# Performance work log

Measured on AMD Instinct MI355X. Metric: run time of the kernel, lower is better.

## Reference

```python
import jax, jax.numpy as jnp
import numpy as np

H = 1024   # hidden size
E = 8      # num experts
B, S = 4, 2048


def setup_inputs() -> dict:
    key = jax.random.key(0)
    k1, k2, k3, k4 = jax.random.split(key, 4)
    x = jax.random.normal(k1, (B, S, H), dtype=jnp.float32)
    wg = jax.random.normal(k2, (H, E), dtype=jnp.float32) * 0.02      # gate weight
    W = jax.random.normal(k3, (E, H, H), dtype=jnp.float32) * 0.02    # expert Linear weights (out, in) per expert
    b = jax.random.normal(k4, (E, H), dtype=jnp.float32) * 0.02       # expert Linear biases
    return {"x": x, "wg": wg, "W": W, "b": b}


def reference(x, wg, W, b):
    Bb, Ss, Hh = x.shape
    Ee = wg.shape[1]
    T = Bb * Ss
    C = T // Ee  # capacity (capacity_factor = 1.0, top-1)

    xt = x.reshape(T, Hh)
    logits = xt @ wg                                   # [T, E]
    probs = jax.nn.softmax(logits, axis=-1)            # [T, E]
    idx = jnp.argmax(probs, axis=-1)                   # [T] top-1 expert
    mask = jax.nn.one_hot(idx, Ee, dtype=xt.dtype)     # [T, E]

    # position of each token within its expert's queue (0-based)
    locations = jnp.cumsum(mask, axis=0) - mask        # [T, E]
    # drop tokens over capacity
    mask = mask * (locations < C).astype(xt.dtype)
    gate = jnp.sum(probs * mask, axis=-1)              # [T] gate prob (0 if dropped)
    loc_s = jnp.sum(locations * mask, axis=-1).astype(jnp.int32)  # [T]
    loc_oh = jax.nn.one_hot(loc_s, C, dtype=xt.dtype)  # [T, C]

    dispatch = mask[:, :, None] * loc_oh[:, None, :]   # [T, E, C]
    combine = gate[:, None, None] * dispatch           # [T, E, C]

    # dispatch tokens -> per-expert buffers [E, C, H]
    exp_in = jnp.einsum('tec,th->ech', dispatch, xt)
    # per-expert Linear: y = x @ W_e^T + b_e
    exp_out = jnp.einsum('ech,efh->ecf', exp_in, W) + b[:, None, :]
    # combine back to tokens, scaled by gate prob
    out = jnp.einsum('tec,ecf->tf', combine, exp_out)  # [T, H]
    return out.reshape(Bb, Ss, Hh)
```

## Files before the change

kernel.cpp:

```cpp
#include <hip/hip_runtime.h>

#define H 1024
#define E 8
#define T 8192
#define CAP 1024

typedef __bf16 bf16x8 __attribute__((ext_vector_type(8)));
typedef float  f32x4  __attribute__((ext_vector_type(4)));
typedef unsigned short u16;

__device__ __forceinline__ u16 f2bf(float f) {
    union { float f; unsigned u; } v; v.f = f;
    unsigned r = v.u + 0x7FFFu + ((v.u >> 16) & 1u);
    return (u16)(r >> 16);
}

typedef __attribute__((address_space(1))) const void* gas_t;
typedef __attribute__((address_space(3))) void* las_t;
__device__ __forceinline__ void gld16(const void* g, void* l) {
    __builtin_amdgcn_global_load_lds((gas_t)g, (las_t)l, 16, 0, 0);
}

__global__ __launch_bounds__(256) void gate_kernel(
    const float* __restrict__ x, const float* __restrict__ wg,
    int* __restrict__ eid, float* __restrict__ gate, u16* __restrict__ xbf) {
    const int wave = (blockIdx.x * blockDim.x + threadIdx.x) >> 6;
    const int lane = threadIdx.x & 63;
    const float* xr = x + (size_t)wave * H;
    float acc[E];
    #pragma unroll
    for (int e = 0; e < E; ++e) acc[e] = 0.f;
    #pragma unroll
    for (int q = 0; q < H / 64; ++q) {
        const int h = q * 64 + lane;
        const float xv = xr[h];
        if (xbf) xbf[(size_t)wave * H + h] = f2bf(xv);
        const float* wr = wg + h * E;
        #pragma unroll
        for (int e = 0; e < E; ++e) acc[e] += xv * wr[e];
    }
    #pragma unroll
    for (int off = 32; off >= 1; off >>= 1) {
        #pragma unroll
        for (int e = 0; e < E; ++e) acc[e] += __shfl_xor(acc[e], off);
    }
    if (lane == 0) {
        float m = acc[0]; int best = 0;
        #pragma unroll
        for (int e = 1; e < E; ++e) if (acc[e] > m) { m = acc[e]; best = e; }
        float s = 0.f;
        #pragma unroll
        for (int e = 0; e < E; ++e) s += expf(acc[e] - m);
        eid[wave]  = best;
        gate[wave] = 1.0f / s;
    }
}

__global__ __launch_bounds__(256) void cvt_kernel(
    const float* __restrict__ src, u16* __restrict__ dst, int n4) {
    int i = blockIdx.x * blockDim.x + threadIdx.x;
    const int stride = gridDim.x * blockDim.x;
    for (; i < n4; i += stride) {
        float4 v = ((const float4*)src)[i];
        ushort4 o;
        o.x = f2bf(v.x); o.y = f2bf(v.y); o.z = f2bf(v.z); o.w = f2bf(v.w);
        ((ushort4*)dst)[i] = o;
    }
}

#define TPT 32
__global__ __launch_bounds__(256) void scan_kernel(
    const int* __restrict__ eid, float* __restrict__ gate,
    int* __restrict__ perm) {
    __shared__ int cnt[256][E];
    __shared__ int base[256][E];
    __shared__ int part[E][8];
    const int tid = threadIdx.x;

    for (int i = tid; i < E * CAP; i += 256) perm[i] = -1;

    const int t0 = tid * TPT;
    int c[E];
    #pragma unroll
    for (int e = 0; e < E; ++e) c[e] = 0;
    for (int i = 0; i < TPT; ++i) {
        const int ei = eid[t0 + i];
        #pragma unroll
        for (int e = 0; e < E; ++e) c[e] += (ei == e);
    }
    #pragma unroll
    for (int e = 0; e < E; ++e) cnt[tid][e] = c[e];
    __syncthreads();
    if (tid < 64) {
        const int e = tid >> 3, j = tid & 7;
        int s = 0;
        for (int i = j * 32; i < j * 32 + 32; ++i) s += cnt[i][e];
        part[e][j] = s;
    }
    __syncthreads();
    if (tid < E) {
        int run = 0;
        #pragma unroll
        for (int j = 0; j < 8; ++j) { int v = part[tid][j]; part[tid][j] = run; run += v; }
    }
    __syncthreads();
    if (tid < 64) {
        const int e = tid >> 3, j = tid & 7;
        int run = part[e][j];
        for (int i = j * 32; i < j * 32 + 32; ++i) { base[i][e] = run; run += cnt[i][e]; }
    }
    __syncthreads();
    #pragma unroll
    for (int e = 0; e < E; ++e) c[e] = base[tid][e];
    for (int i = 0; i < TPT; ++i) {
        const int t = t0 + i;
        const int ei = eid[t];
        int pos = 0;
        #pragma unroll
        for (int e = 0; e < E; ++e) if (ei == e) pos = c[e]++;
        if (pos < CAP) perm[ei * CAP + pos] = t;
        else gate[t] = 0.f;
    }
}

#define BK 64
__global__ __launch_bounds__(256) void moe_gemm_bf(
    const u16* __restrict__ xbf, const u16* __restrict__ Wbf,
    const float* __restrict__ bias, const int* __restrict__ perm,
    const float* __restrict__ gate, float* __restrict__ out) {
    __shared__ __align__(16) u16 As[128 * BK];
    __shared__ __align__(16) u16 Bs[128 * BK];
    __shared__ int   perm_s[128];
    __shared__ float gate_s[128];

    const int e   = blockIdx.z;
    const int mb  = blockIdx.y;
    const int fb  = blockIdx.x;
    const int tid = threadIdx.x;

    if (tid < 128) {
        const int t = perm[e * CAP + mb * 128 + tid];
        perm_s[tid] = t;
        gate_s[tid] = (t >= 0) ? gate[t] : 0.f;
    }
    __syncthreads();

    const int lane = tid & 63;
    const int wv = tid >> 6;
    const int wm = wv >> 1, wn = wv & 1;
    const int l16 = lane & 15, quad = lane >> 4;

    const int rl   = lane >> 3;
    const int cch  = lane & 7;
    const int gch  = cch ^ rl;
    const u16* ga[4]; const u16* gb[4];
    u16* la[4]; u16* lb[4];
    #pragma unroll
    for (int q = 0; q < 4; ++q) {
        const int r = (wv * 4 + q) * 8 + rl;
        const int tA = perm_s[r];
        const int tok = tA >= 0 ? tA : 0;
        ga[q] = xbf + (size_t)tok * H + gch * 8;
        gb[q] = Wbf + (size_t)e * H * H + (size_t)(fb * 128 + r) * H + gch * 8;
        la[q] = &As[(wv * 4 + q) * 512 + lane * 8];
        lb[q] = &Bs[(wv * 4 + q) * 512 + lane * 8];
    }

    f32x4 acc[4][4] = {};

    for (int kt = 0; kt < H / BK; ++kt) {
        __syncthreads();
        #pragma unroll
        for (int q = 0; q < 4; ++q) {
            gld16(ga[q], la[q]);
            gld16(gb[q], lb[q]);
            ga[q] += BK; gb[q] += BK;
        }
        __syncthreads();
        #pragma unroll
        for (int s = 0; s < 2; ++s) {
            bf16x8 af[4], bfr[4];
            const int cc = (s * 4 + quad) ^ (l16 & 7);
            #pragma unroll
            for (int i = 0; i < 4; ++i) {
                af[i]  = *(const bf16x8*)&As[(wm * 64 + i * 16 + l16) * BK + cc * 8];
                bfr[i] = *(const bf16x8*)&Bs[(wn * 64 + i * 16 + l16) * BK + cc * 8];
            }
            #pragma unroll
            for (int mi = 0; mi < 4; ++mi)
                #pragma unroll
                for (int ni = 0; ni < 4; ++ni)
                    acc[mi][ni] = __builtin_amdgcn_mfma_f32_16x16x32_bf16(
                        af[mi], bfr[ni], acc[mi][ni], 0, 0, 0);
        }
    }

    float bv[4];
    #pragma unroll
    for (int ni = 0; ni < 4; ++ni)
        bv[ni] = bias[e * H + fb * 128 + wn * 64 + ni * 16 + l16];

    #pragma unroll
    for (int mi = 0; mi < 4; ++mi) {
        #pragma unroll
        for (int r = 0; r < 4; ++r) {
            const int rowl = wm * 64 + mi * 16 + quad * 4 + r;
            const int t = perm_s[rowl];
            if (t < 0) continue;
            const float g = gate_s[rowl];
            float* orow = out + (size_t)t * H + fb * 128 + wn * 64;
            #pragma unroll
            for (int ni = 0; ni < 4; ++ni)
                orow[ni * 16 + l16] = g * (acc[mi][ni][r] + bv[ni]);
        }
    }
}

#define LDA 40
__global__ __launch_bounds__(256) void moe_gemm_f32(
    const float* __restrict__ x, const float* __restrict__ W,
    const float* __restrict__ bias, const int* __restrict__ perm,
    const float* __restrict__ gate, float* __restrict__ out) {
    __shared__ __align__(16) u16 As[128 * LDA];
    __shared__ __align__(16) u16 Bs[128 * LDA];
    __shared__ int   perm_s[128];
    __shared__ float gate_s[128];

    const int e   = blockIdx.z;
    const int mb  = blockIdx.y;
    const int fb  = blockIdx.x;
    const int tid = threadIdx.x;

    if (tid < 128) {
        const int t = perm[e * CAP + mb * 128 + tid];
        perm_s[tid] = t;
        gate_s[tid] = (t >= 0) ? gate[t] : 0.f;
    }
    __syncthreads();

    const int lane = tid & 63;
    const int wv = tid >> 6;
    const int wm = wv >> 1, wn = wv & 1;
    const int l16 = lane & 15, quad = lane >> 4;

    f32x4 acc[4][4] = {};
    const float* Wbase = W + (size_t)e * H * H + (size_t)(fb * 128) * H;

    for (int kt = 0; kt < H / 32; ++kt) {
        const int k0 = kt * 32;
        __syncthreads();
        #pragma unroll
        for (int p = 0; p < 4; ++p) {
            const int cidx = p * 256 + tid;
            const int row = cidx >> 3;
            const int col = (cidx & 7) * 4;
            const int t = perm_s[row];
            float4 va = (t >= 0) ? *(const float4*)(x + (size_t)t * H + k0 + col)
                                 : make_float4(0.f, 0.f, 0.f, 0.f);
            u16* da = &As[row * LDA + col];
            da[0] = f2bf(va.x); da[1] = f2bf(va.y); da[2] = f2bf(va.z); da[3] = f2bf(va.w);
            float4 vb = *(const float4*)(Wbase + (size_t)row * H + k0 + col);
            u16* db = &Bs[row * LDA + col];
            db[0] = f2bf(vb.x); db[1] = f2bf(vb.y); db[2] = f2bf(vb.z); db[3] = f2bf(vb.w);
        }
        __syncthreads();
        bf16x8 af[4], bfr[4];
        #pragma unroll
        for (int i = 0; i < 4; ++i) {
            af[i]  = *(const bf16x8*)&As[(wm * 64 + i * 16 + l16) * LDA + quad * 8];
            bfr[i] = *(const bf16x8*)&Bs[(wn * 64 + i * 16 + l16) * LDA + quad * 8];
        }
        #pragma unroll
        for (int mi = 0; mi < 4; ++mi)
            #pragma unroll
            for (int ni = 0; ni < 4; ++ni)
                acc[mi][ni] = __builtin_amdgcn_mfma_f32_16x16x32_bf16(
                    af[mi], bfr[ni], acc[mi][ni], 0, 0, 0);
    }

    float bv[4];
    #pragma unroll
    for (int ni = 0; ni < 4; ++ni)
        bv[ni] = bias[e * H + fb * 128 + wn * 64 + ni * 16 + l16];
    #pragma unroll
    for (int mi = 0; mi < 4; ++mi) {
        #pragma unroll
        for (int r = 0; r < 4; ++r) {
            const int rowl = wm * 64 + mi * 16 + quad * 4 + r;
            const int t = perm_s[rowl];
            if (t < 0) continue;
            const float g = gate_s[rowl];
            float* orow = out + (size_t)t * H + fb * 128 + wn * 64;
            #pragma unroll
            for (int ni = 0; ni < 4; ++ni)
                orow[ni * 16 + l16] = g * (acc[mi][ni][r] + bv[ni]);
        }
    }
}

__global__ __launch_bounds__(256) void zero_dropped(
    const float* __restrict__ gate, float* __restrict__ out) {
    const int wave = (blockIdx.x * blockDim.x + threadIdx.x) >> 6;
    const int lane = threadIdx.x & 63;
    if (gate[wave] != 0.f) return;
    float4 z = make_float4(0.f, 0.f, 0.f, 0.f);
    float4* o = (float4*)(out + (size_t)wave * H);
    #pragma unroll
    for (int i = 0; i < H / 4 / 64; ++i) o[i * 64 + lane] = z;
}

extern "C" void kernel_launch(void* const* d_in, const int* in_sizes, int n_in,
                              void* d_out, int out_size, void* d_ws, size_t ws_size,
                              hipStream_t stream) {
    const float* x    = (const float*)d_in[0];
    const float* wg   = (const float*)d_in[1];
    const float* W    = (const float*)d_in[2];
    const float* bias = (const float*)d_in[3];
    float* out = (float*)d_out;

    int*   eid  = (int*)d_ws;
    float* gate = (float*)((char*)d_ws + (size_t)T * 4);
    int*   perm = (int*)((char*)d_ws + (size_t)T * 8);
    u16*   xbf  = (u16*)((char*)d_ws + (size_t)T * 12);
    u16*   Wbf  = xbf + (size_t)T * H;
    const size_t need = (size_t)T * 12 + (size_t)T * H * 2 + (size_t)E * H * H * 2;
    const bool fast = ws_size >= need;

    gate_kernel<<<T / 4, 256, 0, stream>>>(x, wg, eid, gate, fast ? xbf : nullptr);
    if (fast) cvt_kernel<<<2048, 256, 0, stream>>>(W, Wbf, E * H * H / 4);
    scan_kernel<<<1, 256, 0, stream>>>(eid, gate, perm);
    if (fast)
        moe_gemm_bf<<<dim3(8, 8, 8), 256, 0, stream>>>(xbf, Wbf, bias, perm, gate, out);
    else
        moe_gemm_f32<<<dim3(8, 8, 8), 256, 0, stream>>>(x, W, bias, perm, gate, out);
    zero_dropped<<<T / 4, 256, 0, stream>>>(gate, out);
}
```

Measured before the change: 176.8 us.

## Fuse gating and weight conversion into one kernel with LDS-staged gate weights

Merges the gate/x-to-bf16 kernel and the W-to-bf16 conversion kernel into a single launch, with separate block ranges for each job. Gate blocks stage wg in shared memory, each wave processes four tokens with float4 loads, and the eight expert partial sums are reduced with a transpose-style shuffle scheme. The intent is to cut one launch, let the two memory-bound passes overlap, and make the gating loads more efficient. The fp32 fallback GEMM and the workspace-size check are removed, so the code now assumes the workspace is always large enough.

```diff
diff --git a/kernel.cpp b/kernel.cpp
--- a/kernel.cpp
+++ b/kernel.cpp
@@ -21,50 +21,107 @@
     __builtin_amdgcn_global_load_lds((gas_t)g, (las_t)l, 16, 0, 0);
 }
 
-__global__ __launch_bounds__(256) void gate_kernel(
+#define GATE_BLOCKS 512
+#define CVT_BLOCKS  1536
+#define WGP 1028
+
+__global__ __launch_bounds__(256) void gatecvt_kernel(
     const float* __restrict__ x, const float* __restrict__ wg,
-    int* __restrict__ eid, float* __restrict__ gate, u16* __restrict__ xbf) {
-    const int wave = (blockIdx.x * blockDim.x + threadIdx.x) >> 6;
-    const int lane = threadIdx.x & 63;
-    const float* xr = x + (size_t)wave * H;
-    float acc[E];
-    #pragma unroll
-    for (int e = 0; e < E; ++e) acc[e] = 0.f;
-    #pragma unroll
-    for (int q = 0; q < H / 64; ++q) {
-        const int h = q * 64 + lane;
-        const float xv = xr[h];
-        if (xbf) xbf[(size_t)wave * H + h] = f2bf(xv);
-        const float* wr = wg + h * E;
-        #pragma unroll
-        for (int e = 0; e < E; ++e) acc[e] += xv * wr[e];
-    }
-    #pragma unroll
-    for (int off = 32; off >= 1; off >>= 1) {
-        #pragma unroll
-        for (int e = 0; e < E; ++e) acc[e] += __shfl_xor(acc[e], off);
-    }
-    if (lane == 0) {
-        float m = acc[0]; int best = 0;
-        #pragma unroll
-        for (int e = 1; e < E; ++e) if (acc[e] > m) { m = acc[e]; best = e; }
-        float s = 0.f;
-        #pragma unroll
-        for (int e = 0; e < E; ++e) s += expf(acc[e] - m);
-        eid[wave]  = best;
-        gate[wave] = 1.0f / s;
-    }
-}
-
-__global__ __launch_bounds__(256) void cvt_kernel(
-    const float* __restrict__ src, u16* __restrict__ dst, int n4) {
-    int i = blockIdx.x * blockDim.x + threadIdx.x;
-    const int stride = gridDim.x * blockDim.x;
-    for (; i < n4; i += stride) {
-        float4 v = ((const float4*)src)[i];
-        ushort4 o;
-        o.x = f2bf(v.x); o.y = f2bf(v.y); o.z = f2bf(v.z); o.w = f2bf(v.w);
-        ((ushort4*)dst)[i] = o;
+    const float* __restrict__ W,
+    int* __restrict__ eid, float* __restrict__ gate,
+    u16* __restrict__ xbf, u16* __restrict__ Wbf) {
+    __shared__ float wgs[E * WGP];
+    const int tid = threadIdx.x;
+
+    if (blockIdx.x >= GATE_BLOCKS) {
+        int i = (blockIdx.x - GATE_BLOCKS) * 256 + tid;
+        const int n4 = E * H * H / 4;
+        const int stride = CVT_BLOCKS * 256;
+        for (; i < n4; i += stride) {
+            float4 v = ((const float4*)W)[i];
+            ushort4 o;
+            o.x = f2bf(v.x); o.y = f2bf(v.y); o.z = f2bf(v.z); o.w = f2bf(v.w);
+            ((ushort4*)Wbf)[i] = o;
+        }
+        return;
+    }
+
+    for (int i = tid; i < E * H; i += 256)
+        wgs[(i & 7) * WGP + (i >> 3)] = wg[i];
+    __syncthreads();
+
+    const int wv = tid >> 6, lane = tid & 63;
+    const int tbase = blockIdx.x * 16 + wv * 4;
+    const int h00 = lane * 4;
+
+    float a[4][8];
+    #pragma unroll
+    for (int j = 0; j < 4; ++j)
+        #pragma unroll
+        for (int e = 0; e < 8; ++e) a[j][e] = 0.f;
+
+    #pragma unroll
+    for (int q = 0; q < 4; ++q) {
+        const int h0 = q * 256 + h00;
+        float4 xv[4];
+        #pragma unroll
+        for (int j = 0; j < 4; ++j)
+            xv[j] = *(const float4*)(x + (size_t)(tbase + j) * H + h0);
+        #pragma unroll
+        for (int j = 0; j < 4; ++j) {
+            ushort4 o;
+            o.x = f2bf(xv[j].x); o.y = f2bf(xv[j].y);
+            o.z = f2bf(xv[j].z); o.w = f2bf(xv[j].w);
+            *(ushort4*)(xbf + (size_t)(tbase + j) * H + h0) = o;
+        }
+        #pragma unroll
+        for (int e = 0; e < 8; ++e) {
+            const float4 w4 = *(const float4*)&wgs[e * WGP + h0];
+            #pragma unroll
+            for (int j = 0; j < 4; ++j)
+                a[j][e] += xv[j].x * w4.x + xv[j].y * w4.y
+                         + xv[j].z * w4.z + xv[j].w * w4.w;
+        }
+    }
+
+    const bool b0 = lane & 1, b1 = lane & 2, b2 = lane & 4;
+    const int elane = ((lane & 1) << 2) | (lane & 2) | ((lane >> 2) & 1);
+
+    #pragma unroll
+    for (int j = 0; j < 4; ++j) {
+        float* A = a[j];
+        #pragma unroll
+        for (int k = 0; k < 4; ++k) {
+            float t = b0 ? A[k] : A[k + 4];
+            t = __shfl_xor(t, 1);
+            A[k] = (b0 ? A[k + 4] : A[k]) + t;
+        }
+        #pragma unroll
+        for (int k = 0; k < 2; ++k) {
+            float t = b1 ? A[k] : A[k + 2];
+            t = __shfl_xor(t, 2);
+            A[k] = (b1 ? A[k + 2] : A[k]) + t;
+        }
+        {
+            float t = b2 ? A[0] : A[1];
+            t = __shfl_xor(t, 4);
+            A[0] = (b2 ? A[1] : A[0]) + t;
+        }
+        float v = A[0];
+        v += __shfl_xor(v, 8); v += __shfl_xor(v, 16); v += __shfl_xor(v, 32);
+        float m = v; int mi = elane;
+        #pragma unroll
+        for (int off = 1; off <= 4; off <<= 1) {
+            float om = __shfl_xor(m, off);
+            int   oi = __shfl_xor(mi, off);
+            if (om > m || (om == m && oi < mi)) { m = om; mi = oi; }
+        }
+        float s = expf(v - m);
+        s += __shfl_xor(s, 1); s += __shfl_xor(s, 2); s += __shfl_xor(s, 4);
+        if (lane == 0) {
+            eid[tbase + j]  = mi;
+            gate[tbase + j] = 1.0f / s;
+        }
     }
 }
 
@@ -150,9 +207,9 @@
     const int wm = wv >> 1, wn = wv & 1;
     const int l16 = lane & 15, quad = lane >> 4;
 
-    const int rl   = lane >> 3;
-    const int cch  = lane & 7;
-    const int gch  = cch ^ rl;
+    const int rl  = lane >> 3;
+    const int cch = lane & 7;
+    const int gch = cch ^ rl;
     const u16* ga[4]; const u16* gb[4];
     u16* la[4]; u16* lb[4];
     #pragma unroll
@@ -216,88 +273,6 @@
     }
 }
 
-#define LDA 40
-__global__ __launch_bounds__(256) void moe_gemm_f32(
-    const float* __restrict__ x, const float* __restrict__ W,
-    const float* __restrict__ bias, const int* __restrict__ perm,
-    const float* __restrict__ gate, float* __restrict__ out) {
-    __shared__ __align__(16) u16 As[128 * LDA];
-    __shared__ __align__(16) u16 Bs[128 * LDA];
-    __shared__ int   perm_s[128];
-    __shared__ float gate_s[128];
-
-    const int e   = blockIdx.z;
-    const int mb  = blockIdx.y;
-    const int fb  = blockIdx.x;
-    const int tid = threadIdx.x;
-
-    if (tid < 128) {
-        const int t = perm[e * CAP + mb * 128 + tid];
-        perm_s[tid] = t;
-        gate_s[tid] = (t >= 0) ? gate[t] : 0.f;
-    }
-    __syncthreads();
-
-    const int lane = tid & 63;
-    const int wv = tid >> 6;
-    const int wm = wv >> 1, wn = wv & 1;
-    const int l16 = lane & 15, quad = lane >> 4;
-
-    f32x4 acc[4][4] = {};
-    const float* Wbase = W + (size_t)e * H * H + (size_t)(fb * 128) * H;
-
-    for (int kt = 0; kt < H / 32; ++kt) {
-        const int k0 = kt * 32;
-        __syncthreads();
-        #pragma unroll
-        for (int p = 0; p < 4; ++p) {
-            const int cidx = p * 256 + tid;
-            const int row = cidx >> 3;
-            const int col = (cidx & 7) * 4;
-            const int t = perm_s[row];
-            float4 va = (t >= 0) ? *(const float4*)(x + (size_t)t * H + k0 + col)
-                                 : make_float4(0.f, 0.f, 0.f, 0.f);
-            u16* da = &As[row * LDA + col];
-            da[0] = f2bf(va.x); da[1] = f2bf(va.y); da[2] = f2bf(va.z); da[3] = f2bf(va.w);
-            float4 vb = *(const float4*)(Wbase + (size_t)row * H + k0 + col);
-            u16* db = &Bs[row * LDA + col];
-            db[0] = f2bf(vb.x); db[1] = f2bf(vb.y); db[2] = f2bf(vb.z); db[3] = f2bf(vb.w);
-        }
-        __syncthreads();
-        bf16x8 af[4], bfr[4];
-        #pragma unroll
-        for (int i = 0; i < 4; ++i) {
-            af[i]  = *(const bf16x8*)&As[(wm * 64 + i * 16 + l16) * LDA + quad * 8];
-            bfr[i] = *(const bf16x8*)&Bs[(wn * 64 + i * 16 + l16) * LDA + quad * 8];
-        }
-        #pragma unroll
-        for (int mi = 0; mi < 4; ++mi)
-            #pragma unroll
-            for (int ni = 0; ni < 4; ++ni)
-                acc[mi][ni] = __builtin_amdgcn_mfma_f32_16x16x32_bf16(
-                    af[mi], bfr[ni], acc[mi][ni], 0, 0, 0);
-    }
-
-    float bv[4];
-    #pragma unroll
-    for (int ni = 0; ni < 4; ++ni)
-        bv[ni] = bias[e * H + fb * 128 + wn * 64 + ni * 16 + l16];
-    #pragma unroll
-    for (int mi = 0; mi < 4; ++mi) {
-        #pragma unroll
-        for (int r = 0; r < 4; ++r) {
-            const int rowl = wm * 64 + mi * 16 + quad * 4 + r;
-            const int t = perm_s[rowl];
-            if (t < 0) continue;
-            const float g = gate_s[rowl];
-            float* orow = out + (size_t)t * H + fb * 128 + wn * 64;
-            #pragma unroll
-            for (int ni = 0; ni < 4; ++ni)
-                orow[ni * 16 + l16] = g * (acc[mi][ni][r] + bv[ni]);
-        }
-    }
-}
-
 __global__ __launch_bounds__(256) void zero_dropped(
     const float* __restrict__ gate, float* __restrict__ out) {
     const int wave = (blockIdx.x * blockDim.x + threadIdx.x) >> 6;
@@ -323,15 +298,10 @@
     int*   perm = (int*)((char*)d_ws + (size_t)T * 8);
     u16*   xbf  = (u16*)((char*)d_ws + (size_t)T * 12);
     u16*   Wbf  = xbf + (size_t)T * H;
-    const size_t need = (size_t)T * 12 + (size_t)T * H * 2 + (size_t)E * H * H * 2;
-    const bool fast = ws_size >= need;
-
-    gate_kernel<<<T / 4, 256, 0, stream>>>(x, wg, eid, gate, fast ? xbf : nullptr);
-    if (fast) cvt_kernel<<<2048, 256, 0, stream>>>(W, Wbf, E * H * H / 4);
+
+    gatecvt_kernel<<<GATE_BLOCKS + CVT_BLOCKS, 256, 0, stream>>>(
+        x, wg, W, eid, gate, xbf, Wbf);
     scan_kernel<<<1, 256, 0, stream>>>(eid, gate, perm);
-    if (fast)
-        moe_gemm_bf<<<dim3(8, 8, 8), 256, 0, stream>>>(xbf, Wbf, bias, perm, gate, out);
-    else
-        moe_gemm_f32<<<dim3(8, 8, 8), 256, 0, stream>>>(x, W, bias, perm, gate, out);
+    moe_gemm_bf<<<dim3(8, 8, 8), 256, 0, stream>>>(xbf, Wbf, bias, perm, gate, out);
     zero_dropped<<<T / 4, 256, 0, stream>>>(gate, out);
 }
```

New measurement: 156.5 us. -11.5%, faster.
